# Kernel tuning notes

Hardware: AMD Instinct MI355X
Metric: run time of the kernel (lower is better)

Reference implementation:

```python
import jax, jax.numpy as jnp
import numpy as np

VOC_SIZE = 512
CHAR_EMB = 128
N_FILT = 16
KERNELS = [2, 3, 4, 5, 6]
PADS = [0, 0, 1, 2, 3]
B, L = 16384, 32


def _conv1d(x, w, b, pad):
    # x: [B, C, L], w: [O, I, K] -> [B, O, L_out]
    y = jax.lax.conv_general_dilated(
        x, w, window_strides=(1,), padding=[(pad, pad)],
        dimension_numbers=("NCH", "OIH", "NCH"))
    return y + b[None, :, None]


def setup_inputs() -> dict:
    key = jax.random.key(0)
    ks = jax.random.split(key, 12)
    word = jax.random.randint(ks[0], (B, L), 0, VOC_SIZE, dtype=jnp.int64 if jax.config.jax_enable_x64 else jnp.int32)
    emb = jax.random.normal(ks[1], (VOC_SIZE, CHAR_EMB), dtype=jnp.float32) * 0.1
    inp = {"word": word, "emb": emb}
    for i, k in enumerate(KERNELS):
        fan_in = CHAR_EMB * k
        bound = 1.0 / np.sqrt(fan_in)
        inp[f"w{k}"] = jax.random.uniform(ks[2 + 2 * i], (N_FILT, CHAR_EMB, k), jnp.float32, -bound, bound)
        inp[f"b{k}"] = jax.random.uniform(ks[3 + 2 * i], (N_FILT,), jnp.float32, -bound, bound)
    return inp


def reference(word, emb, w2, b2, w3, b3, w4, b4, w5, b5, w6, b6):
    unk = word < 0                      # [B, L]
    idx = jnp.where(unk, 0, word)
    x = emb[idx]                        # [B, L, E]
    x = jnp.where(unk[..., None], 0.0, x)
    x = jnp.transpose(x, (0, 2, 1))     # [B, E, L]
    ws = [w2, w3, w4, w5, w6]
    bs = [b2, b3, b4, b5, b6]
    maxima = [jnp.max(_conv1d(x, w, b, p), axis=-1)
              for w, b, p in zip(ws, bs, PADS)]  # each [B, 16]
    return jnp.concatenate(maxima, axis=-1)      # [B, 80]
```

## Files before the change

### kernel.cpp

```cpp
#include <hip/hip_runtime.h>
#include <hip/hip_fp16.h>

#define VOC    512
#define EMB    128
#define L_SEQ  32
#define NWORDS 16384
#define NCOL   416
#define WPB    128
#define SUBW   32
#define SUBSTRIDE_H 16416
#define SCP    40


__global__ __launch_bounds__(512) void build_pe(
    const float* __restrict__ emb,
    const float* __restrict__ w2, const float* __restrict__ w3,
    const float* __restrict__ w4, const float* __restrict__ w5,
    const float* __restrict__ w6,
    __half* __restrict__ pe)
{
    __shared__ float e[2][EMB];
    const int tid = threadIdx.x;
    const int c0  = blockIdx.x * 2;
    if (tid < 2 * EMB) {
        const int ch = tid >> 7, i = tid & 127, c = c0 + ch;
        e[ch][i] = (c < VOC) ? emb[c * EMB + i] : 0.f;
    }
    __syncthreads();
    const int col = tid;
    if (col >= NCOL) return;

    int k, jpad, base, seg; const float* w;
    if (col < 32)       { k = 2; jpad = 2; base = 0;   seg = 0; w = w2; }
    else if (col < 96)  { k = 3; jpad = 4; base = 32;  seg = 1; w = w3; }
    else if (col < 160) { k = 4; jpad = 4; base = 96;  seg = 2; w = w4; }
    else if (col < 288) { k = 5; jpad = 8; base = 160; seg = 3; w = w5; }
    else                { k = 6; jpad = 8; base = 288; seg = 4; w = w6; }

    const int r  = col - base;
    const int ol = (jpad == 2) ? (r >> 1) : (jpad == 4) ? (r >> 2) : (r >> 3);
    const int j  = r & (jpad - 1);

    int sub, loc;
    if (seg == 0)      { sub = 0;           loc = (ol >> 1) * 4 + j * 2 + (ol & 1); }
    else if (seg == 1) { sub = 1 + (ol>>3); loc = ((ol & 7) >> 1) * 8 + j * 2 + (ol & 1); }
    else if (seg == 2) { sub = 3 + (ol>>3); loc = ((ol & 7) >> 1) * 8 + j * 2 + (ol & 1); }
    else if (seg == 3) { sub = 5 + (ol>>2); loc = (ol & 3) * 8 + j; }
    else               { sub = 9 + (ol>>2); loc = (ol & 3) * 8 + j; }

    float a0 = 0.f, a1 = 0.f;
    if (j < k) {
        const float* wp = w + (ol * EMB) * k + j;
        #pragma unroll 8
        for (int i = 0; i < EMB; ++i) {
            const float wv = wp[i * k];
            a0 += wv * e[0][i]; a1 += wv * e[1][i];
        }
    }
    const int bb = sub * SUBSTRIDE_H + loc;
    pe[bb + c0 * SUBW] = __float2half(a0);
    if (c0 + 1 <= VOC) pe[bb + (c0 + 1) * SUBW] = __float2half(a1);
}

__device__ __forceinline__ float2 h2tof2(int u) {
    return __half22float2(__builtin_bit_cast(__half2, u));
}

template<int K, int PAD>
__device__ __forceinline__ float2 convP(const char* __restrict__ tbl,
                                        const unsigned short* __restrict__ sc,
                                        int w, float2 bias)
{
    constexpr int LOUT = L_SEQ + 2 * PAD - K + 1;
    int d[16];
    {
        const int4* sp = (const int4*)(sc + w * SCP);
        #pragma unroll
        for (int g = 0; g < 4; ++g) {
            const int4 s4 = sp[g];
            d[4*g] = s4.x; d[4*g+1] = s4.y; d[4*g+2] = s4.z; d[4*g+3] = s4.w;
        }
    }
    float2 s[LOUT];
    #pragma unroll
    for (int t = 0; t < LOUT; ++t) s[t] = bias;

    #pragma unroll
    for (int tp = 0; tp < 32; ++tp) {
        const int dw = d[tp >> 1];
        const int pm = (tp & 1) ? (int)(((unsigned)dw) >> 16) : (dw & 0xffff);
        if constexpr (K == 2) {
            const int2 qq = *(const int2*)(tbl + pm);
            const int W2[2] = {qq.x, qq.y};
            #pragma unroll
            for (int j = 0; j < 2; ++j) {
                const int t = tp - j;
                if (t >= 0 && t < LOUT) {
                    const float2 v = h2tof2(W2[j]);
                    s[t].x += v.x; s[t].y += v.y;
                }
            }
        } else {
            const int4 qq = *(const int4*)(tbl + pm);
            const int W4[4] = {qq.x, qq.y, qq.z, qq.w};
            #pragma unroll
            for (int j = 0; j < K; ++j) {
                const int t = tp + PAD - j;
                if (t >= 0 && t < LOUT) {
                    const float2 v = h2tof2(W4[j]);
                    s[t].x += v.x; s[t].y += v.y;
                }
            }
        }
    }
    float2 m = s[0];
    #pragma unroll
    for (int t = 1; t < LOUT; ++t) {
        m.x = fmaxf(m.x, s[t].x); m.y = fmaxf(m.y, s[t].y);
    }
    return m;
}

template<int K, int PAD>
__device__ __forceinline__ float convS(const char* __restrict__ tbl,
                                       const unsigned short* __restrict__ sc,
                                       int w, float bias)
{
    constexpr int LOUT = L_SEQ + 2 * PAD - K + 1;
    int d[16];
    {
        const int4* sp = (const int4*)(sc + w * SCP);
        #pragma unroll
        for (int g = 0; g < 4; ++g) {
            const int4 s4 = sp[g];
            d[4*g] = s4.x; d[4*g+1] = s4.y; d[4*g+2] = s4.z; d[4*g+3] = s4.w;
        }
    }
    float s[LOUT];
    #pragma unroll
    for (int t = 0; t < LOUT; ++t) s[t] = bias;

    #pragma unroll
    for (int tp = 0; tp < 32; ++tp) {
        const int dw = d[tp >> 1];
        const int pm = (tp & 1) ? (int)(((unsigned)dw) >> 16) : (dw & 0xffff);
        const int4 qq = *(const int4*)(tbl + pm);
        const int W4[4] = {qq.x, qq.y, qq.z, qq.w};
        float v[K];
        #pragma unroll
        for (int h = 0; h < (K + 1) / 2; ++h) {
            const float2 f = h2tof2(W4[h]);
            v[2*h] = f.x;
            if (2*h + 1 < K) v[2*h + 1] = f.y;
        }
        #pragma unroll
        for (int j = 0; j < K; ++j) {
            const int t = tp + PAD - j;
            if (t >= 0 && t < LOUT) s[t] += v[j];
        }
    }
    float m = s[0];
    #pragma unroll
    for (int t = 1; t < LOUT; ++t) m = fmaxf(m, s[t]);
    return m;
}

__global__ __launch_bounds__(512, 4) void conv_max(
    const int*    __restrict__ word,
    const __half* __restrict__ pe,
    const float* __restrict__ b2, const float* __restrict__ b3,
    const float* __restrict__ b4, const float* __restrict__ b5,
    const float* __restrict__ b6,
    float*       __restrict__ out)
{
    __shared__ __align__(16) __half tab[513 * 40];
    __shared__ __align__(16) unsigned short sc16[WPB * SCP];

    const int tid = threadIdx.x;
    const int wb  = blockIdx.x & 127;
    const int sub = blockIdx.x >> 7;

    {
        const int4* src = (const int4*)(pe + sub * SUBSTRIDE_H);
        char* tw = (char*)tab;
        for (int i = tid; i < 513 * 4; i += 512)
            *(int4*)(tw + (i >> 2) * 80 + (i & 3) * 16) = src[i];
    }
    {
        const int base = wb * (WPB * L_SEQ);
        #pragma unroll
        for (int r = 0; r < 8; ++r) {
            const int i = tid + r * 512;
            const int c = word[base + i];
            const int ce = (c >= 0) ? c : VOC;
            sc16[(i >> 5) * SCP + (i & 31)] = (unsigned short)(ce * 80);
        }
    }
    __syncthreads();

    const char* tb = (const char*)tab;
    float* ob = out + wb * (WPB * 80);

    if (sub == 0) {
        const int p = tid & 7, w = tid >> 3;
        const char* tbl = tb + p * 8;
        const float2 bias = {b2[2*p], b2[2*p + 1]};
        const float2 ma = convP<2, 0>(tbl, sc16, w,      bias);
        const float2 mb = convP<2, 0>(tbl, sc16, w + 64, bias);
        *(float2*)(ob + w * 80 + 2*p)        = ma;
        *(float2*)(ob + (w + 64) * 80 + 2*p) = mb;
    } else if (sub <= 4) {
        const int fp = tid & 3, w = tid >> 2;
        const char* tbl = tb + fp * 16;
        const int half = (sub - 1) & 1;
        const bool is1 = (sub <= 2);
        const float* bp = is1 ? b3 : b4;
        const int f0 = half * 8 + 2 * fp;
        const float2 bias = {bp[f0], bp[f0 + 1]};
        float2 m;
        if (is1) m = convP<3, 0>(tbl, sc16, w, bias);
        else     m = convP<4, 1>(tbl, sc16, w, bias);
        const int oo = (is1 ? 16 : 32) + f0;
        *(float2*)(ob + w * 80 + oo) = m;
    } else if (sub <= 8) {
        const int ol = tid & 3, w = tid >> 2;
        const char* tbl = tb + ol * 16;
        const int f = (sub - 5) * 4 + ol;
        const float m = convS<5, 2>(tbl, sc16, w, b5[f]);
        ob[w * 80 + 48 + f] = m;
    } else {
        const int ol = tid & 3, w = tid >> 2;
        const char* tbl = tb + ol * 16;
        const int f = (sub - 9) * 4 + ol;
        const float m = convS<6, 3>(tbl, sc16, w, b6[f]);
        ob[w * 80 + 64 + f] = m;
    }
}

extern "C" void kernel_launch(void* const* d_in, const int* in_sizes, int n_in,
                              void* d_out, int out_size, void* d_ws, size_t ws_size,
                              hipStream_t stream)
{
    const int*   word = (const int*)  d_in[0];
    const float* emb  = (const float*)d_in[1];
    const float* w2   = (const float*)d_in[2];
    const float* b2   = (const float*)d_in[3];
    const float* w3   = (const float*)d_in[4];
    const float* b3   = (const float*)d_in[5];
    const float* w4   = (const float*)d_in[6];
    const float* b4   = (const float*)d_in[7];
    const float* w5   = (const float*)d_in[8];
    const float* b5   = (const float*)d_in[9];
    const float* w6   = (const float*)d_in[10];
    const float* b6   = (const float*)d_in[11];
    float* out = (float*)d_out;

    __half* pe16 = (__half*)d_ws;

    build_pe<<<257, 512, 0, stream>>>(emb, w2, w3, w4, w5, w6, pe16);

    conv_max<<<13 * 128, 512, 0, stream>>>(
        word, pe16, b2, b3, b4, b5, b6, out);
}
```

Baseline: 108.3 us.

## Process two word blocks per conv block to amortize table staging

Halves the conv_max grid so each block loads its precomputed half-precision table slice into shared memory once, then handles two 128-word batches in turn, reloading only the word-index buffer between them with barriers. The word-index staging is also vectorized into 128-bit loads and packed 16-bit stores. This cuts redundant table loads from global memory, at the cost of fewer blocks (832) to spread across CUs, less parallelism, and extra synchronization between the two passes.

```diff
diff --git a/kernel.cpp b/kernel.cpp
--- a/kernel.cpp
+++ b/kernel.cpp
@@ -165,6 +165,19 @@
     return m;
 }
 
+__device__ __forceinline__ void sc_write(unsigned short* __restrict__ sc16,
+                                         int tid, int4 a, int4 b)
+{
+    #define ENC(c) ((unsigned)((((c) >= 0) ? (c) : VOC) * 80))
+    int4 o;
+    o.x = (int)(ENC(a.x) | (ENC(a.y) << 16));
+    o.y = (int)(ENC(a.z) | (ENC(a.w) << 16));
+    o.z = (int)(ENC(b.x) | (ENC(b.y) << 16));
+    o.w = (int)(ENC(b.z) | (ENC(b.w) << 16));
+    #undef ENC
+    *(int4*)(sc16 + (tid >> 2) * SCP + (tid & 3) * 8) = o;
+}
+
 __global__ __launch_bounds__(512, 4) void conv_max(
     const int*    __restrict__ word,
     const __half* __restrict__ pe,
@@ -177,8 +190,9 @@
     __shared__ __align__(16) unsigned short sc16[WPB * SCP];
 
     const int tid = threadIdx.x;
-    const int wb  = blockIdx.x & 127;
-    const int sub = blockIdx.x >> 7;
+    const int wbp = blockIdx.x & 63;
+    const int sub = blockIdx.x >> 6;
+    const int wb0 = wbp, wb1 = wbp + 64;
 
     {
         const int4* src = (const int4*)(pe + sub * SUBSTRIDE_H);
@@ -187,28 +201,31 @@
             *(int4*)(tw + (i >> 2) * 80 + (i & 3) * 16) = src[i];
     }
     {
-        const int base = wb * (WPB * L_SEQ);
-        #pragma unroll
-        for (int r = 0; r < 8; ++r) {
-            const int i = tid + r * 512;
-            const int c = word[base + i];
-            const int ce = (c >= 0) ? c : VOC;
-            sc16[(i >> 5) * SCP + (i & 31)] = (unsigned short)(ce * 80);
-        }
+        const int4* wp4 = (const int4*)(word + wb0 * (WPB * L_SEQ)) + tid * 2;
+        sc_write(sc16, tid, wp4[0], wp4[1]);
     }
     __syncthreads();
 
     const char* tb = (const char*)tab;
-    float* ob = out + wb * (WPB * 80);
+    float* ob0 = out + wb0 * (WPB * 80);
+    float* ob1 = out + wb1 * (WPB * 80);
+    const int4* wp1 = (const int4*)(word + wb1 * (WPB * L_SEQ)) + tid * 2;
 
     if (sub == 0) {
         const int p = tid & 7, w = tid >> 3;
         const char* tbl = tb + p * 8;
         const float2 bias = {b2[2*p], b2[2*p + 1]};
-        const float2 ma = convP<2, 0>(tbl, sc16, w,      bias);
-        const float2 mb = convP<2, 0>(tbl, sc16, w + 64, bias);
-        *(float2*)(ob + w * 80 + 2*p)        = ma;
-        *(float2*)(ob + (w + 64) * 80 + 2*p) = mb;
+        float2 ma = convP<2, 0>(tbl, sc16, w,      bias);
+        float2 mb = convP<2, 0>(tbl, sc16, w + 64, bias);
+        *(float2*)(ob0 + w * 80 + 2*p)        = ma;
+        *(float2*)(ob0 + (w + 64) * 80 + 2*p) = mb;
+        __syncthreads();
+        sc_write(sc16, tid, wp1[0], wp1[1]);
+        __syncthreads();
+        ma = convP<2, 0>(tbl, sc16, w,      bias);
+        mb = convP<2, 0>(tbl, sc16, w + 64, bias);
+        *(float2*)(ob1 + w * 80 + 2*p)        = ma;
+        *(float2*)(ob1 + (w + 64) * 80 + 2*p) = mb;
     } else if (sub <= 4) {
         const int fp = tid & 3, w = tid >> 2;
         const char* tbl = tb + fp * 16;
@@ -217,23 +234,41 @@
         const float* bp = is1 ? b3 : b4;
         const int f0 = half * 8 + 2 * fp;
         const float2 bias = {bp[f0], bp[f0 + 1]};
+        const int oo = (is1 ? 16 : 32) + f0;
         float2 m;
         if (is1) m = convP<3, 0>(tbl, sc16, w, bias);
         else     m = convP<4, 1>(tbl, sc16, w, bias);
-        const int oo = (is1 ? 16 : 32) + f0;
-        *(float2*)(ob + w * 80 + oo) = m;
+        *(float2*)(ob0 + w * 80 + oo) = m;
+        __syncthreads();
+        sc_write(sc16, tid, wp1[0], wp1[1]);
+        __syncthreads();
+        if (is1) m = convP<3, 0>(tbl, sc16, w, bias);
+        else     m = convP<4, 1>(tbl, sc16, w, bias);
+        *(float2*)(ob1 + w * 80 + oo) = m;
     } else if (sub <= 8) {
         const int ol = tid & 3, w = tid >> 2;
         const char* tbl = tb + ol * 16;
         const int f = (sub - 5) * 4 + ol;
-        const float m = convS<5, 2>(tbl, sc16, w, b5[f]);
-        ob[w * 80 + 48 + f] = m;
+        const float bias = b5[f];
+        float m = convS<5, 2>(tbl, sc16, w, bias);
+        ob0[w * 80 + 48 + f] = m;
+        __syncthreads();
+        sc_write(sc16, tid, wp1[0], wp1[1]);
+        __syncthreads();
+        m = convS<5, 2>(tbl, sc16, w, bias);
+        ob1[w * 80 + 48 + f] = m;
     } else {
         const int ol = tid & 3, w = tid >> 2;
         const char* tbl = tb + ol * 16;
         const int f = (sub - 9) * 4 + ol;
-        const float m = convS<6, 3>(tbl, sc16, w, b6[f]);
-        ob[w * 80 + 64 + f] = m;
+        const float bias = b6[f];
+        float m = convS<6, 3>(tbl, sc16, w, bias);
+        ob0[w * 80 + 64 + f] = m;
+        __syncthreads();
+        sc_write(sc16, tid, wp1[0], wp1[1]);
+        __syncthreads();
+        m = convS<6, 3>(tbl, sc16, w, bias);
+        ob1[w * 80 + 64 + f] = m;
     }
 }
 
@@ -259,6 +294,6 @@
 
     build_pe<<<257, 512, 0, stream>>>(emb, w2, w3, w4, w5, w6, pe16);
 
-    conv_max<<<13 * 128, 512, 0, stream>>>(
+    conv_max<<<13 * 64, 512, 0, stream>>>(
         word, pe16, b2, b3, b4, b5, b6, out);
 }
```

After: 109.4 us. No clear change (+1.0%).

## Repack k=2 table into 4-filter groups, stream max, vectorize word load, reverse block order

Applied to the files above, without the earlier changes.

Changes the precomputed k=2 table layout so each thread reads a 16-byte entry that covers four filters and two taps. A new streaming routine keeps only two running partial sums per filter pair and takes the max as it goes, instead of holding a full array of outputs per word. The word-index staging now uses two int4 loads per thread with packed 16-bit writes, and the block-to-sub-table mapping is reversed so the heavier k=5/6 blocks launch first. The convS unpack is simplified. This changes the k=2 thread mapping and makes the staging code assume aligned vector loads.

```diff
diff --git a/kernel.cpp b/kernel.cpp
--- a/kernel.cpp
+++ b/kernel.cpp
@@ -42,7 +42,7 @@
     const int j  = r & (jpad - 1);
 
     int sub, loc;
-    if (seg == 0)      { sub = 0;           loc = (ol >> 1) * 4 + j * 2 + (ol & 1); }
+    if (seg == 0)      { sub = 0;           loc = (ol >> 2) * 8 + j * 4 + (ol & 3); }
     else if (seg == 1) { sub = 1 + (ol>>3); loc = ((ol & 7) >> 1) * 8 + j * 2 + (ol & 1); }
     else if (seg == 2) { sub = 3 + (ol>>3); loc = ((ol & 7) >> 1) * 8 + j * 2 + (ol & 1); }
     else if (seg == 3) { sub = 5 + (ol>>2); loc = (ol & 3) * 8 + j; }
@@ -66,6 +66,50 @@
     return __half22float2(__builtin_bit_cast(__half2, u));
 }
 
+__device__ __forceinline__ void sc_load(const unsigned short* __restrict__ sc,
+                                        int w, int* __restrict__ d)
+{
+    const int4* sp = (const int4*)(sc + w * SCP);
+    #pragma unroll
+    for (int g = 0; g < 4; ++g) {
+        const int4 s4 = sp[g];
+        d[4*g] = s4.x; d[4*g+1] = s4.y; d[4*g+2] = s4.z; d[4*g+3] = s4.w;
+    }
+}
+
+__device__ __forceinline__ void convQ2(const char* __restrict__ tbl,
+                                       const unsigned short* __restrict__ sc,
+                                       int w, float2 ba, float2 bb,
+                                       float2* __restrict__ mA,
+                                       float2* __restrict__ mB)
+{
+    int d[16];
+    sc_load(sc, w, d);
+    float2 rA[2], rB[2];
+    float2 xA = make_float2(-3.0e38f, -3.0e38f), xB = xA;
+
+    #pragma unroll
+    for (int tp = 0; tp < 32; ++tp) {
+        const int dw = d[tp >> 1];
+        const int pm = (tp & 1) ? (int)(((unsigned)dw) >> 16) : (dw & 0xffff);
+        const int4 qq = *(const int4*)(tbl + pm);
+        const int cur = tp & 1, prv = cur ^ 1;
+        if (tp < 31) {
+            const float2 v0 = h2tof2(qq.x), v1 = h2tof2(qq.y);
+            rA[cur] = make_float2(ba.x + v0.x, ba.y + v0.y);
+            rB[cur] = make_float2(bb.x + v1.x, bb.y + v1.y);
+        }
+        if (tp > 0) {
+            const float2 u0 = h2tof2(qq.z), u1 = h2tof2(qq.w);
+            rA[prv].x += u0.x; rA[prv].y += u0.y;
+            rB[prv].x += u1.x; rB[prv].y += u1.y;
+            xA.x = fmaxf(xA.x, rA[prv].x); xA.y = fmaxf(xA.y, rA[prv].y);
+            xB.x = fmaxf(xB.x, rB[prv].x); xB.y = fmaxf(xB.y, rB[prv].y);
+        }
+    }
+    *mA = xA; *mB = xB;
+}
+
 template<int K, int PAD>
 __device__ __forceinline__ float2 convP(const char* __restrict__ tbl,
                                         const unsigned short* __restrict__ sc,
@@ -73,70 +117,8 @@
 {
     constexpr int LOUT = L_SEQ + 2 * PAD - K + 1;
     int d[16];
-    {
-        const int4* sp = (const int4*)(sc + w * SCP);
-        #pragma unroll
-        for (int g = 0; g < 4; ++g) {
-            const int4 s4 = sp[g];
-            d[4*g] = s4.x; d[4*g+1] = s4.y; d[4*g+2] = s4.z; d[4*g+3] = s4.w;
-        }
-    }
+    sc_load(sc, w, d);
     float2 s[LOUT];
-    #pragma unroll
-    for (int t = 0; t < LOUT; ++t) s[t] = bias;
-
-    #pragma unroll
-    for (int tp = 0; tp < 32; ++tp) {
-        const int dw = d[tp >> 1];
-        const int pm = (tp & 1) ? (int)(((unsigned)dw) >> 16) : (dw & 0xffff);
-        if constexpr (K == 2) {
-            const int2 qq = *(const int2*)(tbl + pm);
-            const int W2[2] = {qq.x, qq.y};
-            #pragma unroll
-            for (int j = 0; j < 2; ++j) {
-                const int t = tp - j;
-                if (t >= 0 && t < LOUT) {
-                    const float2 v = h2tof2(W2[j]);
-                    s[t].x += v.x; s[t].y += v.y;
-                }
-            }
-        } else {
-            const int4 qq = *(const int4*)(tbl + pm);
-            const int W4[4] = {qq.x, qq.y, qq.z, qq.w};
-            #pragma unroll
-            for (int j = 0; j < K; ++j) {
-                const int t = tp + PAD - j;
-                if (t >= 0 && t < LOUT) {
-                    const float2 v = h2tof2(W4[j]);
-                    s[t].x += v.x; s[t].y += v.y;
-                }
-            }
-        }
-    }
-    float2 m = s[0];
-    #pragma unroll
-    for (int t = 1; t < LOUT; ++t) {
-        m.x = fmaxf(m.x, s[t].x); m.y = fmaxf(m.y, s[t].y);
-    }
-    return m;
-}
-
-template<int K, int PAD>
-__device__ __forceinline__ float convS(const char* __restrict__ tbl,
-                                       const unsigned short* __restrict__ sc,
-                                       int w, float bias)
-{
-    constexpr int LOUT = L_SEQ + 2 * PAD - K + 1;
-    int d[16];
-    {
-        const int4* sp = (const int4*)(sc + w * SCP);
-        #pragma unroll
-        for (int g = 0; g < 4; ++g) {
-            const int4 s4 = sp[g];
-            d[4*g] = s4.x; d[4*g+1] = s4.y; d[4*g+2] = s4.z; d[4*g+3] = s4.w;
-        }
-    }
-    float s[LOUT];
     #pragma unroll
     for (int t = 0; t < LOUT; ++t) s[t] = bias;
 
@@ -146,12 +128,45 @@
         const int pm = (tp & 1) ? (int)(((unsigned)dw) >> 16) : (dw & 0xffff);
         const int4 qq = *(const int4*)(tbl + pm);
         const int W4[4] = {qq.x, qq.y, qq.z, qq.w};
+        #pragma unroll
+        for (int j = 0; j < K; ++j) {
+            const int t = tp + PAD - j;
+            if (t >= 0 && t < LOUT) {
+                const float2 v = h2tof2(W4[j]);
+                s[t].x += v.x; s[t].y += v.y;
+            }
+        }
+    }
+    float2 m = s[0];
+    #pragma unroll
+    for (int t = 1; t < LOUT; ++t) {
+        m.x = fmaxf(m.x, s[t].x); m.y = fmaxf(m.y, s[t].y);
+    }
+    return m;
+}
+
+template<int K, int PAD>
+__device__ __forceinline__ float convS(const char* __restrict__ tbl,
+                                       const unsigned short* __restrict__ sc,
+                                       int w, float bias)
+{
+    constexpr int LOUT = L_SEQ + 2 * PAD - K + 1;
+    int d[16];
+    sc_load(sc, w, d);
+    float s[LOUT];
+    #pragma unroll
+    for (int t = 0; t < LOUT; ++t) s[t] = bias;
+
+    #pragma unroll
+    for (int tp = 0; tp < 32; ++tp) {
+        const int dw = d[tp >> 1];
+        const int pm = (tp & 1) ? (int)(((unsigned)dw) >> 16) : (dw & 0xffff);
+        const int4 qq = *(const int4*)(tbl + pm);
         float v[K];
-        #pragma unroll
-        for (int h = 0; h < (K + 1) / 2; ++h) {
-            const float2 f = h2tof2(W4[h]);
-            v[2*h] = f.x;
-            if (2*h + 1 < K) v[2*h + 1] = f.y;
+        {
+            const float2 f0 = h2tof2(qq.x), f1 = h2tof2(qq.y), f2 = h2tof2(qq.z);
+            v[0] = f0.x; v[1] = f0.y; v[2] = f1.x; v[3] = f1.y; v[4] = f2.x;
+            if constexpr (K >= 6) v[5] = f2.y;
         }
         #pragma unroll
         for (int j = 0; j < K; ++j) {
@@ -163,6 +178,19 @@
     #pragma unroll
     for (int t = 1; t < LOUT; ++t) m = fmaxf(m, s[t]);
     return m;
+}
+
+__device__ __forceinline__ void sc_write(unsigned short* __restrict__ sc16,
+                                         int tid, int4 a, int4 b)
+{
+    #define ENC(c) ((unsigned)((((c) >= 0) ? (c) : VOC) * 80))
+    int4 o;
+    o.x = (int)(ENC(a.x) | (ENC(a.y) << 16));
+    o.y = (int)(ENC(a.z) | (ENC(a.w) << 16));
+    o.z = (int)(ENC(b.x) | (ENC(b.y) << 16));
+    o.w = (int)(ENC(b.z) | (ENC(b.w) << 16));
+    #undef ENC
+    *(int4*)(sc16 + (tid >> 2) * SCP + (tid & 3) * 8) = o;
 }
 
 __global__ __launch_bounds__(512, 4) void conv_max(
@@ -178,7 +206,7 @@
 
     const int tid = threadIdx.x;
     const int wb  = blockIdx.x & 127;
-    const int sub = blockIdx.x >> 7;
+    const int sub = 12 - (blockIdx.x >> 7);
 
     {
         const int4* src = (const int4*)(pe + sub * SUBSTRIDE_H);
@@ -187,51 +215,43 @@
             *(int4*)(tw + (i >> 2) * 80 + (i & 3) * 16) = src[i];
     }
     {
-        const int base = wb * (WPB * L_SEQ);
-        #pragma unroll
-        for (int r = 0; r < 8; ++r) {
-            const int i = tid + r * 512;
-            const int c = word[base + i];
-            const int ce = (c >= 0) ? c : VOC;
-            sc16[(i >> 5) * SCP + (i & 31)] = (unsigned short)(ce * 80);
-        }
+        const int4* wp4 = (const int4*)(word + wb * (WPB * L_SEQ)) + tid * 2;
+        sc_write(sc16, tid, wp4[0], wp4[1]);
     }
     __syncthreads();
 
     const char* tb = (const char*)tab;
     float* ob = out + wb * (WPB * 80);
+    const int q = tid & 3, w = tid >> 2;
 
     if (sub == 0) {
-        const int p = tid & 7, w = tid >> 3;
-        const char* tbl = tb + p * 8;
-        const float2 bias = {b2[2*p], b2[2*p + 1]};
-        const float2 ma = convP<2, 0>(tbl, sc16, w,      bias);
-        const float2 mb = convP<2, 0>(tbl, sc16, w + 64, bias);
-        *(float2*)(ob + w * 80 + 2*p)        = ma;
-        *(float2*)(ob + (w + 64) * 80 + 2*p) = mb;
+        const char* tbl = tb + q * 16;
+        const float2 ba = {b2[4*q],     b2[4*q + 1]};
+        const float2 bb = {b2[4*q + 2], b2[4*q + 3]};
+        float2 mA, mB;
+        convQ2(tbl, sc16, w, ba, bb, &mA, &mB);
+        float4 o4; o4.x = mA.x; o4.y = mA.y; o4.z = mB.x; o4.w = mB.y;
+        *(float4*)(ob + w * 80 + 4*q) = o4;
     } else if (sub <= 4) {
-        const int fp = tid & 3, w = tid >> 2;
-        const char* tbl = tb + fp * 16;
+        const char* tbl = tb + q * 16;
         const int half = (sub - 1) & 1;
         const bool is1 = (sub <= 2);
         const float* bp = is1 ? b3 : b4;
-        const int f0 = half * 8 + 2 * fp;
+        const int f0 = half * 8 + 2 * q;
         const float2 bias = {bp[f0], bp[f0 + 1]};
+        const int oo = (is1 ? 16 : 32) + f0;
         float2 m;
         if (is1) m = convP<3, 0>(tbl, sc16, w, bias);
         else     m = convP<4, 1>(tbl, sc16, w, bias);
-        const int oo = (is1 ? 16 : 32) + f0;
         *(float2*)(ob + w * 80 + oo) = m;
     } else if (sub <= 8) {
-        const int ol = tid & 3, w = tid >> 2;
-        const char* tbl = tb + ol * 16;
-        const int f = (sub - 5) * 4 + ol;
+        const char* tbl = tb + q * 16;
+        const int f = (sub - 5) * 4 + q;
         const float m = convS<5, 2>(tbl, sc16, w, b5[f]);
         ob[w * 80 + 48 + f] = m;
     } else {
-        const int ol = tid & 3, w = tid >> 2;
-        const char* tbl = tb + ol * 16;
-        const int f = (sub - 9) * 4 + ol;
+        const char* tbl = tb + q * 16;
+        const int f = (sub - 9) * 4 + q;
         const float m = convS<6, 3>(tbl, sc16, w, b6[f]);
         ob[w * 80 + 64 + f] = m;
     }
```

Result: slower. 122.2 us (+12.9%).
